# Kernel tuning notes

Hardware: AMD Instinct MI355X
Metric: run time of the kernel (lower is better)

Reference implementation:

```python
import jax, jax.numpy as jnp
import numpy as np

QMIN, QMAX = 0, 255        # 8-bit asymmetric activation quant bounds
GROUP_SIZE = 128

def setup_inputs() -> dict:
    key = jax.random.key(0)
    k1, k2, k3, k4, k5 = jax.random.split(key, 5)
    x = jax.random.normal(k1, (1, 2048, 4096), dtype=jnp.float32)
    qweight = jax.random.randint(k2, (4096, 32, 128), 0, 16, dtype=jnp.int32)  # uint4 codes
    w_scales = jax.random.uniform(k3, (4096, 32), dtype=jnp.float32, minval=0.001, maxval=0.02)
    w_zero_points = jax.random.randint(k4, (4096, 32), 0, 16, dtype=jnp.int32)
    bias = jax.random.normal(k5, (4096,), dtype=jnp.float32)
    return {"x": x, "qweight": qweight, "w_scales": w_scales,
            "w_zero_points": w_zero_points, "bias": bias}

def reference(x, qweight, w_scales, w_zero_points, bias):
    xf = x.astype(jnp.float32)
    # per-token (last-dim) asymmetric dynamic activation quantization
    xmin = jnp.min(xf, axis=-1, keepdims=True)
    xmax = jnp.max(xf, axis=-1, keepdims=True)
    x_scale = jnp.clip((xmax - xmin) / (QMAX - QMIN), 1e-5, None)
    x_zp = jnp.clip(jnp.round(-xmin / x_scale), QMIN, QMAX)
    q = jnp.clip(jnp.round(xf / x_scale) + x_zp, QMIN, QMAX)
    centered_x = (q - x_zp).reshape(*x.shape[:-1], -1, GROUP_SIZE)  # [B,S,G,C]
    # grouped weight dequant (zero-point centered)
    centered_w = qweight.astype(jnp.float32) - w_zero_points.astype(jnp.float32)[..., None]  # [O,G,C]
    acc = jnp.einsum('bsgc,ogc->bsog', centered_x, centered_w)  # [B,S,O,G]
    out = (acc * w_scales[None, None]).sum(axis=-1)  # apply per-group weight scales
    out = out * x_scale  # per-token activation scale
    out = out + bias
    return out
```

## Files before the change

### kernel.cpp

```cpp
#include <hip/hip_runtime.h>
#include <hip/hip_bf16.h>
#include <stdint.h>

#define M_DIM 2048
#define N_DIM 4096
#define K_DIM 4096
#define NGROUP 32
#define GSIZE 128

#define BM 128
#define BN 64
#define BKB 128

#define RQ_UP   (127.0f / 15.0f)
#define RQ_DOWN (15.0f / 127.0f)

typedef __attribute__((ext_vector_type(4))) int   int32x4_t;
typedef __attribute__((ext_vector_type(4))) float f32x4_t;

static __device__ __forceinline__ void gl2lds16(const void* g, void* l) {
    auto gp = (const __attribute__((address_space(1))) unsigned int*)(uintptr_t)g;
    auto lp = (__attribute__((address_space(3))) unsigned int*)(uintptr_t)l;
    __builtin_amdgcn_global_load_lds(gp, lp, 16, 0, 0);
}

__global__ __launch_bounds__(256) void sn_kernel(
        const float* __restrict__ wsc, float* __restrict__ rsn,
        float* __restrict__ fws)
{
    const int n = blockIdx.x * 256 + threadIdx.x;
    const float4* w4 = (const float4*)(wsc + (size_t)n * NGROUP);
    float s = 0.f;
#pragma unroll
    for (int p = 0; p < 8; ++p) {
        float4 w = w4[p];
        s = fmaxf(s, fmaxf(fmaxf(w.x, w.y), fmaxf(w.z, w.w)));
    }
    rsn[n] = RQ_UP / s;
    fws[n] = s * RQ_DOWN;
}

#define QUANT_BLOCKS M_DIM
#define DEQ_BLOCKS ((N_DIM * K_DIM) / 8 / 256)

__global__ __launch_bounds__(256) void prep_kernel(
        const float* __restrict__ x,
        const int* __restrict__ qw,
        const float* __restrict__ wsc,
        const int* __restrict__ wzp,
        const float* __restrict__ rsn,
        char* __restrict__ A8,
        char* __restrict__ Bt8,
        float* __restrict__ xscale,
        float* __restrict__ xzpc,
        int* __restrict__ Sw)
{
    const int t = threadIdx.x;
    if (blockIdx.x < QUANT_BLOCKS) {
        const int s = blockIdx.x;
        const float* xrow = x + (size_t)s * K_DIM;

        float xv[16];
        float vmin = 1e38f, vmax = -1e38f;
#pragma unroll
        for (int p = 0; p < 4; ++p) {
            float4 v = *((const float4*)(xrow + p * 1024) + t);
            xv[p*4+0] = v.x; xv[p*4+1] = v.y; xv[p*4+2] = v.z; xv[p*4+3] = v.w;
            vmin = fminf(vmin, fminf(fminf(v.x, v.y), fminf(v.z, v.w)));
            vmax = fmaxf(vmax, fmaxf(fmaxf(v.x, v.y), fmaxf(v.z, v.w)));
        }
#pragma unroll
        for (int off = 32; off > 0; off >>= 1) {
            vmin = fminf(vmin, __shfl_xor(vmin, off));
            vmax = fmaxf(vmax, __shfl_xor(vmax, off));
        }
        __shared__ float smin[4], smax[4];
        const int wave = t >> 6;
        if ((t & 63) == 0) { smin[wave] = vmin; smax[wave] = vmax; }
        __syncthreads();
        vmin = fminf(fminf(smin[0], smin[1]), fminf(smin[2], smin[3]));
        vmax = fmaxf(fmaxf(smax[0], smax[1]), fmaxf(smax[2], smax[3]));

        float sc = (vmax - vmin) / 255.0f;
        sc = fmaxf(sc, 1e-5f);
        float zp = rintf(-vmin / sc);
        zp = fminf(fmaxf(zp, 0.0f), 255.0f);

#pragma unroll
        for (int p = 0; p < 4; ++p) {
            int b[4];
#pragma unroll
            for (int e = 0; e < 4; ++e) {
                float q = fminf(fmaxf(rintf(xv[p*4+e] / sc) + zp, 0.0f), 255.0f);
                b[e] = (int)q - 128;
            }
            unsigned pack = (b[0] & 0xff) | ((b[1] & 0xff) << 8) |
                            ((b[2] & 0xff) << 16) | ((b[3] & 0xff) << 24);
            *(unsigned*)(A8 + (size_t)s * K_DIM + p * 1024 + t * 4) = pack;
        }
        if (t == 0) { xscale[s] = sc; xzpc[s] = 128.0f - zp; }
    } else {
        const size_t base = ((size_t)(blockIdx.x - QUANT_BLOCKS) * 256 + t) * 8;
        const int n = (int)(base >> 12);
        const int g = (int)((base >> 7) & 31);
        const int zp = wzp[n * NGROUP + g];
        const float factor = wsc[n * NGROUP + g] * rsn[n];

        int4 c0 = *(const int4*)(qw + base);
        int4 c1 = *(const int4*)(qw + base + 4);
        int w[8];
        w[0] = (int)rintf((float)(c0.x - zp) * factor);
        w[1] = (int)rintf((float)(c0.y - zp) * factor);
        w[2] = (int)rintf((float)(c0.z - zp) * factor);
        w[3] = (int)rintf((float)(c0.w - zp) * factor);
        w[4] = (int)rintf((float)(c1.x - zp) * factor);
        w[5] = (int)rintf((float)(c1.y - zp) * factor);
        w[6] = (int)rintf((float)(c1.z - zp) * factor);
        w[7] = (int)rintf((float)(c1.w - zp) * factor);
        uint2 pk;
        pk.x = (w[0] & 0xff) | ((w[1] & 0xff) << 8) | ((w[2] & 0xff) << 16) | ((w[3] & 0xff) << 24);
        pk.y = (w[4] & 0xff) | ((w[5] & 0xff) << 8) | ((w[6] & 0xff) << 16) | ((w[7] & 0xff) << 24);
        *(uint2*)(Bt8 + base) = pk;

        int s8 = w[0] + w[1] + w[2] + w[3] + w[4] + w[5] + w[6] + w[7];
#pragma unroll
        for (int off = 1; off < 16; off <<= 1) s8 += __shfl_xor(s8, off);
        if ((t & 15) == 0)
            Sw[n * NGROUP + g] = s8;
    }
}

__global__ __launch_bounds__(256) void ws_kernel(
        const float* __restrict__ fws, const int* __restrict__ Sw,
        float* __restrict__ WSf)
{
    const int n = blockIdx.x * 256 + threadIdx.x;
    const int4* s4 = (const int4*)(Sw + (size_t)n * NGROUP);
    int acc = 0;
#pragma unroll
    for (int p = 0; p < 8; ++p) {
        int4 s = s4[p];
        acc += s.x + s.y + s.z + s.w;
    }
    WSf[n] = fws[n] * (float)acc;
}

__global__ __launch_bounds__(256, 3) void gemm_kernel(
        const char* __restrict__ A8,
        const char* __restrict__ Bt8,
        const float* __restrict__ xscale,
        const float* __restrict__ xzpc,
        const float* __restrict__ fws,
        const float* __restrict__ WSf,
        const float* __restrict__ bias,
        float* __restrict__ out)
{
    __shared__ __align__(16) char As[2][BM * BKB];
    __shared__ __align__(16) char Bs[2][BN * BKB];

    const int tid  = threadIdx.x;
    const int bm   = blockIdx.y;
    const int bn   = blockIdx.x;
    const int wave = tid >> 6;
    const int lane = tid & 63;
    const int wr   = (wave >> 1) * 64;
    const int wc   = (wave & 1) * 32;
    const int lrow  = lane & 15;
    const int lquad = lane >> 4;
    const int l7    = lrow & 7;

    const int srow8 = lane >> 3;
    const int cdat  = (lane & 7) ^ srow8;

    int32x4_t iacc[4][2];
    const int32x4_t zi = {0, 0, 0, 0};
#pragma unroll
    for (int i = 0; i < 4; ++i)
#pragma unroll
        for (int j = 0; j < 2; ++j) iacc[i][j] = zi;

    const char* Ab = A8  + (size_t)(bm * BM) * K_DIM;
    const char* Bb = Bt8 + (size_t)(bn * BN) * K_DIM;
    const int n0 = bn * BN;
    const int ncol0 = n0 + wc + 0  + lrow;
    const int ncol1 = n0 + wc + 16 + lrow;

#pragma unroll
    for (int p = 0; p < 4; ++p) {
        const int rbase = (p * 4 + wave) * 8;
        gl2lds16(Ab + (size_t)(rbase + srow8) * K_DIM + cdat * 16,
                 As[0] + rbase * BKB);
    }
#pragma unroll
    for (int p = 0; p < 2; ++p) {
        const int rbase = (p * 4 + wave) * 8;
        gl2lds16(Bb + (size_t)(rbase + srow8) * K_DIM + cdat * 16,
                 Bs[0] + rbase * BKB);
    }

    for (int kt = 0; kt < K_DIM / GSIZE; ++kt) {
        const int cur = kt & 1;
        __syncthreads();

        if (kt < 31) {
            const int k0 = (kt + 1) * GSIZE;
#pragma unroll
            for (int p = 0; p < 4; ++p) {
                const int rbase = (p * 4 + wave) * 8;
                gl2lds16(Ab + (size_t)(rbase + srow8) * K_DIM + k0 + cdat * 16,
                         As[cur ^ 1] + rbase * BKB);
            }
#pragma unroll
            for (int p = 0; p < 2; ++p) {
                const int rbase = (p * 4 + wave) * 8;
                gl2lds16(Bb + (size_t)(rbase + srow8) * K_DIM + k0 + cdat * 16,
                         Bs[cur ^ 1] + rbase * BKB);
            }
        }

#pragma unroll
        for (int ks = 0; ks < 2; ++ks) {
            const int kc = ks * 4 + lquad;
            int32x4_t af[4], bf[2];
#pragma unroll
            for (int i = 0; i < 4; ++i)
                af[i] = *(const int32x4_t*)(As[cur] + (wr + i * 16 + lrow) * BKB + ((kc ^ l7) * 16));
#pragma unroll
            for (int j = 0; j < 2; ++j)
                bf[j] = *(const int32x4_t*)(Bs[cur] + (wc + j * 16 + lrow) * BKB + ((kc ^ l7) * 16));
#pragma unroll
            for (int i = 0; i < 4; ++i)
#pragma unroll
                for (int j = 0; j < 2; ++j)
                    iacc[i][j] = __builtin_amdgcn_mfma_i32_16x16x64_i8(
                        af[i], bf[j], iacc[i][j], 0, 0, 0);
        }
    }

    const int m0 = bm * BM + wr;
    const float fn0 = fws[ncol0], wf0 = WSf[ncol0], bb0 = bias[ncol0];
    const float fn1 = fws[ncol1], wf1 = WSf[ncol1], bb1 = bias[ncol1];
#pragma unroll
    for (int i = 0; i < 4; ++i) {
#pragma unroll
        for (int r = 0; r < 4; ++r) {
            const int m = m0 + i * 16 + lquad * 4 + r;
            const float xs  = xscale[m];
            const float czp = xzpc[m];
            out[(size_t)m * N_DIM + ncol0] =
                xs * (fn0 * (float)iacc[i][0][r] + czp * wf0) + bb0;
            out[(size_t)m * N_DIM + ncol1] =
                xs * (fn1 * (float)iacc[i][1][r] + czp * wf1) + bb1;
        }
    }
}

extern "C" void kernel_launch(void* const* d_in, const int* in_sizes, int n_in,
                              void* d_out, int out_size, void* d_ws, size_t ws_size,
                              hipStream_t stream) {
    const float* x     = (const float*)d_in[0];
    const int*   qw    = (const int*)d_in[1];
    const float* wsc   = (const float*)d_in[2];
    const int*   wzp   = (const int*)d_in[3];
    const float* bias  = (const float*)d_in[4];
    float* out = (float*)d_out;

    char* A8  = (char*)d_ws;
    char* Bt8 = A8 + (size_t)M_DIM * K_DIM;
    float* xscale = (float*)(Bt8 + (size_t)N_DIM * K_DIM);
    float* xzpc   = xscale + M_DIM;
    int*   Sw     = (int*)(xzpc + M_DIM);
    float* rsn    = (float*)(Sw + (size_t)N_DIM * NGROUP);
    float* fws    = rsn + N_DIM;
    float* WSf    = fws + N_DIM;

    sn_kernel<<<N_DIM / 256, 256, 0, stream>>>(wsc, rsn, fws);
    prep_kernel<<<QUANT_BLOCKS + DEQ_BLOCKS, 256, 0, stream>>>(
        x, qw, wsc, wzp, rsn, A8, Bt8, xscale, xzpc, Sw);
    ws_kernel<<<N_DIM / 256, 256, 0, stream>>>(fws, Sw, WSf);
    dim3 grid(N_DIM / BN, M_DIM / BM);
    gemm_kernel<<<grid, 256, 0, stream>>>(A8, Bt8, xscale, xzpc, fws, WSf, bias, out);
}
```

Baseline: 180.0 us.

## Enlarge GEMM tiles with 4-stage LDS pipeline and fold scale kernels into others

The GEMM now uses 256x128 tiles with 512 threads and a four-slot, 64-byte K-slice pipeline. It waits on vmcnt explicitly and raises wave priority around the MFMA block, so global-to-LDS loads stay in flight longer and each tile gets more reuse. The small sn_kernel and ws_kernel launches are removed. The per-row weight-scale max is recomputed in prep via shuffles, and fws/WSf are computed per block in GEMM shared memory. This trades launch overhead and bandwidth for more LDS and registers per block, fewer blocks (256 total), and some redundant reductions.

```diff
diff --git a/kernel.cpp b/kernel.cpp
--- a/kernel.cpp
+++ b/kernel.cpp
@@ -1,5 +1,4 @@
 #include <hip/hip_runtime.h>
-#include <hip/hip_bf16.h>
 #include <stdint.h>
 
 #define M_DIM 2048
@@ -8,15 +7,17 @@
 #define NGROUP 32
 #define GSIZE 128
 
-#define BM 128
-#define BN 64
-#define BKB 128
-
 #define RQ_UP   (127.0f / 15.0f)
 #define RQ_DOWN (15.0f / 127.0f)
 
-typedef __attribute__((ext_vector_type(4))) int   int32x4_t;
-typedef __attribute__((ext_vector_type(4))) float f32x4_t;
+#define BM 256
+#define BN 128
+#define KSLICE 64
+#define NSLICE (K_DIM / KSLICE)
+#define ASLOT (BM * KSLICE)
+#define BSLOT (BN * KSLICE)
+
+typedef __attribute__((ext_vector_type(4))) int int32x4_t;
 
 static __device__ __forceinline__ void gl2lds16(const void* g, void* l) {
     auto gp = (const __attribute__((address_space(1))) unsigned int*)(uintptr_t)g;
@@ -24,21 +25,9 @@
     __builtin_amdgcn_global_load_lds(gp, lp, 16, 0, 0);
 }
 
-__global__ __launch_bounds__(256) void sn_kernel(
-        const float* __restrict__ wsc, float* __restrict__ rsn,
-        float* __restrict__ fws)
-{
-    const int n = blockIdx.x * 256 + threadIdx.x;
-    const float4* w4 = (const float4*)(wsc + (size_t)n * NGROUP);
-    float s = 0.f;
-#pragma unroll
-    for (int p = 0; p < 8; ++p) {
-        float4 w = w4[p];
-        s = fmaxf(s, fmaxf(fmaxf(w.x, w.y), fmaxf(w.z, w.w)));
-    }
-    rsn[n] = RQ_UP / s;
-    fws[n] = s * RQ_DOWN;
-}
+#define WAITVM_(N) asm volatile("s_waitcnt vmcnt(" #N ")" ::: "memory")
+#define WAITVM(N) WAITVM_(N)
+#define BARRIER() asm volatile("s_barrier" ::: "memory")
 
 #define QUANT_BLOCKS M_DIM
 #define DEQ_BLOCKS ((N_DIM * K_DIM) / 8 / 256)
@@ -48,7 +37,6 @@
         const int* __restrict__ qw,
         const float* __restrict__ wsc,
         const int* __restrict__ wzp,
-        const float* __restrict__ rsn,
         char* __restrict__ A8,
         char* __restrict__ Bt8,
         float* __restrict__ xscale,
@@ -104,7 +92,14 @@
         const int n = (int)(base >> 12);
         const int g = (int)((base >> 7) & 31);
         const int zp = wzp[n * NGROUP + g];
-        const float factor = wsc[n * NGROUP + g] * rsn[n];
+
+        const int cl = t & 15;
+        float2 wp = *(const float2*)(wsc + (size_t)n * NGROUP + cl * 2);
+        float smx = fmaxf(wp.x, wp.y);
+#pragma unroll
+        for (int off = 1; off < 16; off <<= 1)
+            smx = fmaxf(smx, __shfl_xor(smx, off));
+        const float factor = wsc[n * NGROUP + g] * (RQ_UP / smx);
 
         int4 c0 = *(const int4*)(qw + base);
         int4 c1 = *(const int4*)(qw + base + 4);
@@ -130,116 +125,128 @@
     }
 }
 
-__global__ __launch_bounds__(256) void ws_kernel(
-        const float* __restrict__ fws, const int* __restrict__ Sw,
-        float* __restrict__ WSf)
-{
-    const int n = blockIdx.x * 256 + threadIdx.x;
-    const int4* s4 = (const int4*)(Sw + (size_t)n * NGROUP);
-    int acc = 0;
-#pragma unroll
-    for (int p = 0; p < 8; ++p) {
-        int4 s = s4[p];
-        acc += s.x + s.y + s.z + s.w;
-    }
-    WSf[n] = fws[n] * (float)acc;
-}
-
-__global__ __launch_bounds__(256, 3) void gemm_kernel(
+__global__ __launch_bounds__(512, 2) void gemm_kernel(
         const char* __restrict__ A8,
         const char* __restrict__ Bt8,
         const float* __restrict__ xscale,
         const float* __restrict__ xzpc,
-        const float* __restrict__ fws,
-        const float* __restrict__ WSf,
+        const float* __restrict__ wsc,
+        const int* __restrict__ Sw,
         const float* __restrict__ bias,
         float* __restrict__ out)
 {
-    __shared__ __align__(16) char As[2][BM * BKB];
-    __shared__ __align__(16) char Bs[2][BN * BKB];
+    __shared__ __align__(16) char As[4][ASLOT];
+    __shared__ __align__(16) char Bs[4][BSLOT];
+    __shared__ float fws_s[BN], wsf_s[BN];
 
     const int tid  = threadIdx.x;
+    const int bn   = blockIdx.x;
     const int bm   = blockIdx.y;
-    const int bn   = blockIdx.x;
     const int wave = tid >> 6;
     const int lane = tid & 63;
-    const int wr   = (wave >> 1) * 64;
-    const int wc   = (wave & 1) * 32;
+    const int wr   = wave >> 1;
+    const int wcl  = wave & 1;
     const int lrow  = lane & 15;
     const int lquad = lane >> 4;
-    const int l7    = lrow & 7;
-
-    const int srow8 = lane >> 3;
-    const int cdat  = (lane & 7) ^ srow8;
-
-    int32x4_t iacc[4][2];
-    const int32x4_t zi = {0, 0, 0, 0};
-#pragma unroll
-    for (int i = 0; i < 4; ++i)
-#pragma unroll
-        for (int j = 0; j < 2; ++j) iacc[i][j] = zi;
+
+    if (tid < BN) {
+        const int n = bn * BN + tid;
+        const int4* s4 = (const int4*)(Sw + (size_t)n * NGROUP);
+        int acc = 0;
+#pragma unroll
+        for (int p = 0; p < 8; ++p) { int4 v = s4[p]; acc += v.x + v.y + v.z + v.w; }
+        const float4* w4 = (const float4*)(wsc + (size_t)n * NGROUP);
+        float s = 0.f;
+#pragma unroll
+        for (int p = 0; p < 8; ++p) {
+            float4 w = w4[p];
+            s = fmaxf(s, fmaxf(fmaxf(w.x, w.y), fmaxf(w.z, w.w)));
+        }
+        const float fw = s * RQ_DOWN;
+        fws_s[tid] = fw;
+        wsf_s[tid] = fw * (float)acc;
+    }
+    asm volatile("s_waitcnt vmcnt(0) lgkmcnt(0)" ::: "memory");
+    BARRIER();
 
     const char* Ab = A8  + (size_t)(bm * BM) * K_DIM;
     const char* Bb = Bt8 + (size_t)(bn * BN) * K_DIM;
-    const int n0 = bn * BN;
-    const int ncol0 = n0 + wc + 0  + lrow;
-    const int ncol1 = n0 + wc + 16 + lrow;
-
-#pragma unroll
-    for (int p = 0; p < 4; ++p) {
-        const int rbase = (p * 4 + wave) * 8;
-        gl2lds16(Ab + (size_t)(rbase + srow8) * K_DIM + cdat * 16,
-                 As[0] + rbase * BKB);
-    }
-#pragma unroll
-    for (int p = 0; p < 2; ++p) {
-        const int rbase = (p * 4 + wave) * 8;
-        gl2lds16(Bb + (size_t)(rbase + srow8) * K_DIM + cdat * 16,
-                 Bs[0] + rbase * BKB);
-    }
-
-    for (int kt = 0; kt < K_DIM / GSIZE; ++kt) {
-        const int cur = kt & 1;
-        __syncthreads();
-
-        if (kt < 31) {
-            const int k0 = (kt + 1) * GSIZE;
-#pragma unroll
-            for (int p = 0; p < 4; ++p) {
-                const int rbase = (p * 4 + wave) * 8;
-                gl2lds16(Ab + (size_t)(rbase + srow8) * K_DIM + k0 + cdat * 16,
-                         As[cur ^ 1] + rbase * BKB);
-            }
-#pragma unroll
-            for (int p = 0; p < 2; ++p) {
-                const int rbase = (p * 4 + wave) * 8;
-                gl2lds16(Bb + (size_t)(rbase + srow8) * K_DIM + k0 + cdat * 16,
-                         Bs[cur ^ 1] + rbase * BKB);
-            }
-        }
-
-#pragma unroll
-        for (int ks = 0; ks < 2; ++ks) {
-            const int kc = ks * 4 + lquad;
-            int32x4_t af[4], bf[2];
-#pragma unroll
-            for (int i = 0; i < 4; ++i)
-                af[i] = *(const int32x4_t*)(As[cur] + (wr + i * 16 + lrow) * BKB + ((kc ^ l7) * 16));
-#pragma unroll
-            for (int j = 0; j < 2; ++j)
-                bf[j] = *(const int32x4_t*)(Bs[cur] + (wc + j * 16 + lrow) * BKB + ((kc ^ l7) * 16));
-#pragma unroll
-            for (int i = 0; i < 4; ++i)
-#pragma unroll
-                for (int j = 0; j < 2; ++j)
-                    iacc[i][j] = __builtin_amdgcn_mfma_i32_16x16x64_i8(
-                        af[i], bf[j], iacc[i][j], 0, 0, 0);
-        }
-    }
-
-    const int m0 = bm * BM + wr;
-    const float fn0 = fws[ncol0], wf0 = WSf[ncol0], bb0 = bias[ncol0];
-    const float fn1 = fws[ncol1], wf1 = WSf[ncol1], bb1 = bias[ncol1];
+    const int lsub = lane >> 2;
+    const int csrc = (lane & 3) ^ ((lane >> 3) & 3);
+    const char* gA0 = Ab + (size_t)((wave      ) * 16 + lsub) * K_DIM + csrc * 16;
+    const char* gA1 = Ab + (size_t)((wave + 8  ) * 16 + lsub) * K_DIM + csrc * 16;
+    const char* gB0 = Bb + (size_t)((wave      ) * 16 + lsub) * K_DIM + csrc * 16;
+    const int lA0 = wave * 1024;
+    const int lA1 = 8192 + wave * 1024;
+    const int lB0 = wave * 1024;
+
+    const int xq = (lquad ^ ((lrow >> 1) & 3)) * 16;
+    int aoff[4], boff[4];
+#pragma unroll
+    for (int i = 0; i < 4; ++i)
+        aoff[i] = (wr * 64 + i * 16 + lrow) * KSLICE + xq;
+#pragma unroll
+    for (int j = 0; j < 4; ++j)
+        boff[j] = (wcl * 64 + j * 16 + lrow) * KSLICE + xq;
+
+    int32x4_t iacc[4][4];
+    const int32x4_t zi = {0, 0, 0, 0};
+#pragma unroll
+    for (int i = 0; i < 4; ++i)
+#pragma unroll
+        for (int j = 0; j < 4; ++j) iacc[i][j] = zi;
+
+#define STAGE(t) {                                                   \
+        const int sl_ = (t) & 3;                                     \
+        const size_t k0_ = (size_t)(t) * KSLICE;                     \
+        gl2lds16(gA0 + k0_, &As[sl_][0] + lA0);                      \
+        gl2lds16(gA1 + k0_, &As[sl_][0] + lA1);                      \
+        gl2lds16(gB0 + k0_, &Bs[sl_][0] + lB0);                      \
+    }
+
+#define SLICE(s, VMN) {                                              \
+        if ((s) + 3 < NSLICE) STAGE((s) + 3);                        \
+        WAITVM(VMN);                                                 \
+        BARRIER();                                                   \
+        const char* Ap_ = &As[(s) & 3][0];                           \
+        const char* Bp_ = &Bs[(s) & 3][0];                           \
+        int32x4_t af_[4], bf_[4];                                    \
+        _Pragma("unroll")                                            \
+        for (int i_ = 0; i_ < 4; ++i_)                               \
+            af_[i_] = *(const int32x4_t*)(Ap_ + aoff[i_]);           \
+        _Pragma("unroll")                                            \
+        for (int j_ = 0; j_ < 4; ++j_)                               \
+            bf_[j_] = *(const int32x4_t*)(Bp_ + boff[j_]);           \
+        __builtin_amdgcn_s_setprio(1);                               \
+        _Pragma("unroll")                                            \
+        for (int i_ = 0; i_ < 4; ++i_)                               \
+            _Pragma("unroll")                                        \
+            for (int j_ = 0; j_ < 4; ++j_)                           \
+                iacc[i_][j_] = __builtin_amdgcn_mfma_i32_16x16x64_i8(\
+                    af_[i_], bf_[j_], iacc[i_][j_], 0, 0, 0);        \
+        __builtin_amdgcn_s_setprio(0);                               \
+        BARRIER();                                                   \
+    }
+
+    STAGE(0); STAGE(1); STAGE(2);
+
+    for (int s = 0; s < NSLICE - 3; ++s)
+        SLICE(s, 9);
+    SLICE(NSLICE - 3, 6);
+    SLICE(NSLICE - 2, 3);
+    SLICE(NSLICE - 1, 0);
+
+    float fn[4], wf[4], bb[4];
+    int ncol[4];
+#pragma unroll
+    for (int j = 0; j < 4; ++j) {
+        const int ncl = wcl * 64 + j * 16 + lrow;
+        ncol[j] = bn * BN + ncl;
+        fn[j] = fws_s[ncl];
+        wf[j] = wsf_s[ncl];
+        bb[j] = bias[ncol[j]];
+    }
+    const int m0 = bm * BM + wr * 64;
 #pragma unroll
     for (int i = 0; i < 4; ++i) {
 #pragma unroll
@@ -247,12 +254,14 @@
             const int m = m0 + i * 16 + lquad * 4 + r;
             const float xs  = xscale[m];
             const float czp = xzpc[m];
-            out[(size_t)m * N_DIM + ncol0] =
-                xs * (fn0 * (float)iacc[i][0][r] + czp * wf0) + bb0;
-            out[(size_t)m * N_DIM + ncol1] =
-                xs * (fn1 * (float)iacc[i][1][r] + czp * wf1) + bb1;
-        }
-    }
+            float* orow = out + (size_t)m * N_DIM;
+#pragma unroll
+            for (int j = 0; j < 4; ++j)
+                orow[ncol[j]] = xs * (fn[j] * (float)iacc[i][j][r] + czp * wf[j]) + bb[j];
+        }
+    }
+#undef SLICE
+#undef STAGE
 }
 
 extern "C" void kernel_launch(void* const* d_in, const int* in_sizes, int n_in,
@@ -270,14 +279,9 @@
     float* xscale = (float*)(Bt8 + (size_t)N_DIM * K_DIM);
     float* xzpc   = xscale + M_DIM;
     int*   Sw     = (int*)(xzpc + M_DIM);
-    float* rsn    = (float*)(Sw + (size_t)N_DIM * NGROUP);
-    float* fws    = rsn + N_DIM;
-    float* WSf    = fws + N_DIM;
-
-    sn_kernel<<<N_DIM / 256, 256, 0, stream>>>(wsc, rsn, fws);
+
     prep_kernel<<<QUANT_BLOCKS + DEQ_BLOCKS, 256, 0, stream>>>(
-        x, qw, wsc, wzp, rsn, A8, Bt8, xscale, xzpc, Sw);
-    ws_kernel<<<N_DIM / 256, 256, 0, stream>>>(fws, Sw, WSf);
+        x, qw, wsc, wzp, A8, Bt8, xscale, xzpc, Sw);
     dim3 grid(N_DIM / BN, M_DIM / BM);
-    gemm_kernel<<<grid, 256, 0, stream>>>(A8, Bt8, xscale, xzpc, fws, WSf, bias, out);
-}
+    gemm_kernel<<<grid, 512, 0, stream>>>(A8, Bt8, xscale, xzpc, wsc, Sw, bias, out);
+}
```

Measured after the change: 173.8 us. 3.5% less time.
